# Kernel tuning notes

Hardware: AMD Instinct MI355X
Metric: run time of the kernel (lower is better)

The kernel has to match this reference:

```python
import jax, jax.numpy as jnp
import numpy as np

Q_DIM = 1024
KV_DIM = 1024
D_ATTN = 1024
N_HEADS = 16
HDIM = D_ATTN // N_HEADS
LOOKBACK = 3
KW = LOOKBACK + 1
SCALE = HDIM ** -0.5

B, LQ, LKV = 4, 4096, 512


def setup_inputs() -> dict:
    key = jax.random.key(0)
    ks = jax.random.split(key, 6)
    q = jax.random.normal(ks[0], (B, LQ, Q_DIM), dtype=jnp.float32)
    kv_src = jax.random.normal(ks[1], (B, LKV, KV_DIM), dtype=jnp.float32)
    seg_id = jnp.sort(jax.random.randint(ks[2], (B, LQ), 0, LKV), axis=-1)
    # Linear weights (torch convention: y = x @ W.T), no bias
    Wq = jax.random.normal(ks[3], (D_ATTN, Q_DIM), dtype=jnp.float32) * (Q_DIM ** -0.5)
    Wkv = jax.random.normal(ks[4], (2 * D_ATTN, KV_DIM), dtype=jnp.float32) * (KV_DIM ** -0.5)
    Wo = jax.random.normal(ks[5], (Q_DIM, D_ATTN), dtype=jnp.float32) * (D_ATTN ** -0.5)
    return {"q": q, "kv_src": kv_src, "seg_id": seg_id, "Wq": Wq, "Wkv": Wkv, "Wo": Wo}


def _split_heads(x):
    # (B, L, D) -> (B, H, L, Dh)
    b, l, _ = x.shape
    return x.reshape(b, l, N_HEADS, HDIM).transpose(0, 2, 1, 3)


def reference(q, kv_src, seg_id, Wq, Wkv, Wo):
    b, lq, _ = q.shape
    lkv = kv_src.shape[1]

    qh = _split_heads(q @ Wq.T)                      # (B,H,Lq,Dh)
    kv = kv_src @ Wkv.T                              # (B,Lkv,2*D)
    k, v = jnp.split(kv, 2, axis=-1)
    kh = _split_heads(k)                             # (B,H,Lkv,Dh)
    vh = _split_heads(v)

    offsets = jnp.arange(KW)                         # (Kw,)
    gather = seg_id[:, :, None] - offsets            # (B,Lq,Kw)
    neg_mask = gather < 0
    gc = jnp.clip(gather, 0, lkv - 1)                # (B,Lq,Kw)

    b_idx = jnp.arange(b)[:, None, None]
    # advanced indexing: (B,Lq,Kw,H,Dh) -> transpose to (B,H,Lq,Kw,Dh)
    k_sel = kh[b_idx, :, gc].transpose(0, 3, 1, 2, 4)
    v_sel = vh[b_idx, :, gc].transpose(0, 3, 1, 2, 4)

    scores = jnp.einsum('bhqd,bhqkd->bhqk', qh, k_sel) * SCALE
    neg_inf = jnp.finfo(scores.dtype).min
    scores = jnp.where(neg_mask[:, None, :, :], neg_inf, scores)
    probs = jax.nn.softmax(scores, axis=-1)
    out = jnp.einsum('bhqk,bhqkd->bhqd', probs, v_sel)   # (B,H,Lq,Dh)
    out = out.transpose(0, 2, 1, 3).reshape(b, lq, D_ATTN)
    return out @ Wo.T                                # (B,Lq,q_dim)
```

## Files before the change

### kernel.cpp

```cpp
#include <hip/hip_runtime.h>
#include <math.h>

#define NH 16
#define HDIM 64
#define D_ATTN 1024
#define KW 4
#define ATT_SCALE 0.125f
#define LKV_C 512
#define LQ_C 4096
#define B_C 4

typedef _Float16 f16;
typedef _Float16 f16x8 __attribute__((ext_vector_type(8)));
typedef _Float16 f16x4 __attribute__((ext_vector_type(4)));
typedef float f32x4 __attribute__((ext_vector_type(4)));

typedef __attribute__((address_space(3))) unsigned int as3_uint;
typedef __attribute__((address_space(1))) const unsigned int as1_uint;

__device__ __forceinline__ void gld_lds16(const f16* g, f16* l) {
    __builtin_amdgcn_global_load_lds((as1_uint*)g, (as3_uint*)l, 16, 0, 0);
}

__global__ __launch_bounds__(256) void split_hi(const float* __restrict__ x,
                                                f16* __restrict__ hi, int n4) {
    int i = blockIdx.x * 256 + threadIdx.x;
    if (i >= n4) return;
    float4 v = ((const float4*)x)[i];
    ((f16x4*)hi)[i] = (f16x4){(f16)v.x, (f16)v.y, (f16)v.z, (f16)v.w};
}

template <typename OT>
__global__ __launch_bounds__(256) void gemm_f16(const f16* __restrict__ A,
                                                const f16* __restrict__ B,
                                                OT* __restrict__ C,
                                                int M, int N, int K) {
    __shared__ f16 smem[2 * 128 * 32];
    f16* sA = smem;
    f16* sB = smem + 4096;

    const int t = threadIdx.x;
    const int w = t >> 6;
    const int lane = t & 63;
    const int bm = blockIdx.y * 128;
    const int bn = blockIdx.x * 128;
    const int wm = (w & 1) * 64;
    const int wn = (w >> 1) * 64;

    f32x4 acc[4][4] = {};

    const int frow = lane & 15;
    const int fchunk = lane >> 4;

    const int srow = t >> 2;
    const int chunk = (t & 3) ^ ((t >> 3) & 3);
    const size_t aoff0 = (size_t)(bm + srow) * K + chunk * 8;
    const size_t aoff1 = (size_t)(bm + 64 + srow) * K + chunk * 8;
    const size_t boff0 = (size_t)(bn + srow) * K + chunk * 8;
    const size_t boff1 = (size_t)(bn + 64 + srow) * K + chunk * 8;
    const unsigned loff0 = (w * 64) * 8;
    const unsigned loff1 = (256 + w * 64) * 8;

    gld_lds16(A + aoff0, sA + loff0);  gld_lds16(A + aoff1, sA + loff1);
    gld_lds16(B + boff0, sB + loff0);  gld_lds16(B + boff1, sB + loff1);

    for (int k0 = 0; k0 < K; k0 += 32) {
        __syncthreads();

        f16x8 a[4], b[4];
        #pragma unroll
        for (int i = 0; i < 4; ++i) {
            const int r = wm + i * 16 + frow;
            a[i] = *(const f16x8*)(sA + r * 32 + (fchunk ^ ((r >> 1) & 3)) * 8);
        }
        #pragma unroll
        for (int j = 0; j < 4; ++j) {
            const int r = wn + j * 16 + frow;
            b[j] = *(const f16x8*)(sB + r * 32 + (fchunk ^ ((r >> 1) & 3)) * 8);
        }

        __syncthreads();

        if (k0 + 32 < K) {
            const int kn = k0 + 32;
            gld_lds16(A + aoff0 + kn, sA + loff0);  gld_lds16(A + aoff1 + kn, sA + loff1);
            gld_lds16(B + boff0 + kn, sB + loff0);  gld_lds16(B + boff1 + kn, sB + loff1);
        }

        #pragma unroll
        for (int i = 0; i < 4; ++i)
            #pragma unroll
            for (int j = 0; j < 4; ++j)
                acc[i][j] = __builtin_amdgcn_mfma_f32_16x16x32_f16(a[i], b[j], acc[i][j], 0, 0, 0);
    }

    const int rbase = bm + wm + (lane >> 4) * 4;
    const int cbase = bn + wn + (lane & 15);
    #pragma unroll
    for (int i = 0; i < 4; ++i)
        #pragma unroll
        for (int j = 0; j < 4; ++j)
            #pragma unroll
            for (int r = 0; r < 4; ++r)
                C[(size_t)(rbase + i * 16 + r) * N + cbase + j * 16] = (OT)acc[i][j][r];
}

__device__ __forceinline__ void stage_half(const f16* __restrict__ g, size_t row0,
                                           int K, int kcol, f16* l) {
    const int t = threadIdx.x;
    #pragma unroll
    for (int i = 0; i < 2; ++i) {
        const int idx = i * 512 + t;
        const int r = idx >> 3;
        const int qg = (idx & 7) ^ (r & 7);
        gld_lds16(g + (row0 + r) * (size_t)K + kcol + qg * 8, l + idx * 8);
    }
}

#define BAR __builtin_amdgcn_s_barrier()
#define VM6 asm volatile("s_waitcnt vmcnt(6)" ::: "memory")
#define VM8 asm volatile("s_waitcnt vmcnt(8)" ::: "memory")
#define VM0 asm volatile("s_waitcnt vmcnt(0)" ::: "memory")

#define RD_A(S, mh)                                                         \
    { _Pragma("unroll") for (int mi = 0; mi < 4; ++mi) {                    \
        const f16* p = (S) + ((mh) * 128 + mi * 32 + arow) * 64;            \
        a[0][mi] = *(const f16x8*)(p + q0);                                 \
        a[1][mi] = *(const f16x8*)(p + q1); } }

#define RD_B(S, nh)                                                         \
    { _Pragma("unroll") for (int ni = 0; ni < 2; ++ni) {                    \
        const f16* p = (S) + (((nh) * 2 + ni) * 64 + brow) * 64;            \
        b[0][(nh) * 2 + ni] = *(const f16x8*)(p + q0);                      \
        b[1][(nh) * 2 + ni] = *(const f16x8*)(p + q1); } }

#define QUAD(mh, nh)                                                        \
    { __builtin_amdgcn_s_setprio(1);                                        \
      _Pragma("unroll") for (int mi = 0; mi < 4; ++mi)                      \
      _Pragma("unroll") for (int ni = 0; ni < 2; ++ni) {                    \
          f32x4& c = acc[(mh) * 4 + mi][(nh) * 2 + ni];                     \
          c = __builtin_amdgcn_mfma_f32_16x16x32_f16(a[0][mi], b[0][(nh) * 2 + ni], c, 0, 0, 0); \
          c = __builtin_amdgcn_mfma_f32_16x16x32_f16(a[1][mi], b[1][(nh) * 2 + ni], c, 0, 0, 0); \
      }                                                                     \
      __builtin_amdgcn_s_setprio(0); }

template <typename OT>
__global__ __launch_bounds__(512, 2) void gemm256(const f16* __restrict__ A,
                                                  const f16* __restrict__ B,
                                                  OT* __restrict__ C,
                                                  int M, int N, int K) {
    __shared__ __align__(16) f16 smem[4 * 16384];
    f16* const sA0 = smem;
    f16* const sA1 = smem + 16384;
    f16* const sB0 = smem + 32768;
    f16* const sB1 = smem + 49152;

    const int t = threadIdx.x;
    const int lane = t & 63;
    const int w = t >> 6;
    const int wr = w >> 2;
    const int wc = w & 3;
    const int frow = lane & 15;
    const int fc = lane >> 4;

    const int nbx = N >> 8;
    const int nwg = gridDim.x;
    const int wg = (blockIdx.x & 7) * (nwg >> 3) + (blockIdx.x >> 3);
    const int bm = (wg / nbx) << 8;
    const int bn = (wg % nbx) << 8;

    const int arow = wr * 16 + frow;
    const int brow = wc * 16 + frow;
    const int q0 = (fc ^ (frow & 7)) * 8;
    const int q1 = ((4 + fc) ^ (frow & 7)) * 8;

    f32x4 acc[8][4] = {};
    f16x8 a[2][4], b[2][4];

    stage_half(A, bm,       K, 0,  sA0);
    stage_half(B, bn,       K, 0,  sB0);
    stage_half(B, bn + 128, K, 0,  sB0 + 8192);
    stage_half(A, bm + 128, K, 0,  sA0 + 8192);
    stage_half(A, bm,       K, 64, sA1);
    stage_half(B, bn,       K, 64, sB1);
    stage_half(B, bn + 128, K, 64, sB1 + 8192);
    stage_half(A, bm + 128, K, 64, sA1 + 8192);
    VM8;
    BAR;

    const int NT = K >> 7;
    for (int it = 0; it < NT; ++it) {
        const bool lastit = (it == NT - 1);
        const int kc2 = (it * 2 + 2) << 6;
        const int kc3 = (it * 2 + 3) << 6;

        RD_A(sA0, 0); RD_B(sB0, 0);
        BAR; QUAD(0, 0); BAR;
        RD_B(sB0, 1);
        if (!lastit) { stage_half(A, bm, K, kc2, sA0); stage_half(B, bn, K, kc2, sB0); }
        BAR; QUAD(0, 1); BAR;
        RD_A(sA0, 1);
        if (!lastit) stage_half(B, bn + 128, K, kc2, sB0 + 8192);
        BAR; QUAD(1, 0); BAR;
        if (lastit) { VM0; } else { VM6; stage_half(A, bm + 128, K, kc2, sA0 + 8192); }
        BAR; QUAD(1, 1); BAR;

        RD_A(sA1, 0); RD_B(sB1, 0);
        BAR; QUAD(0, 0); BAR;
        RD_B(sB1, 1);
        if (!lastit) { stage_half(A, bm, K, kc3, sA1); stage_half(B, bn, K, kc3, sB1); }
        BAR; QUAD(0, 1); BAR;
        RD_A(sA1, 1);
        if (!lastit) stage_half(B, bn + 128, K, kc3, sB1 + 8192);
        BAR; QUAD(1, 0); BAR;
        if (!lastit) { VM6; stage_half(A, bm + 128, K, kc3, sA1 + 8192); }
        BAR; QUAD(1, 1); BAR;
    }

    const size_t rb = (size_t)bm + wr * 16 + ((lane >> 4) << 2);
    const int cb = bn + wc * 16 + (lane & 15);
    #pragma unroll
    for (int m = 0; m < 8; ++m)
        #pragma unroll
        for (int n = 0; n < 4; ++n)
            #pragma unroll
            for (int rr = 0; rr < 4; ++rr)
                C[(rb + m * 32 + rr) * N + cb + n * 64] = (OT)acc[m][n][rr];
}

__global__ __launch_bounds__(256) void attn_kernel(const f16* __restrict__ qh,
                                                   const f16* __restrict__ kvp,
                                                   const int* __restrict__ seg_id,
                                                   f16* __restrict__ attn_o) {
    const int hg = threadIdx.x >> 6;
    const int lane = threadIdx.x & 63;
    const int r0 = blockIdx.x << 2;
    const int hh = lane >> 4;
    const int s  = lane & 15;
    const int dbase = (hg * 4 + hh) * HDIM + 4 * s;
    const int b = r0 >> 12;
    const f16* kvb = kvp + (size_t)b * LKV_C * (2 * D_ATTN);

    int seg[4];
    float4 q[4];
    #pragma unroll
    for (int i = 0; i < 4; ++i) {
        seg[i] = seg_id[r0 + i];
        f16x4 qv = *(const f16x4*)(qh + (size_t)(r0 + i) * D_ATTN + dbase);
        q[i] = make_float4((float)qv.x, (float)qv.y, (float)qv.z, (float)qv.w);
    }

    float sc[4][KW];
    #pragma unroll
    for (int i = 0; i < 4; ++i)
        #pragma unroll
        for (int w = 0; w < KW; ++w) {
            const int j = seg[i] - w;
            float p = 0.f;
            if (j >= 0) {
                f16x4 k4 = *(const f16x4*)(kvb + (size_t)j * (2 * D_ATTN) + dbase);
                p = q[i].x * (float)k4.x + q[i].y * (float)k4.y +
                    q[i].z * (float)k4.z + q[i].w * (float)k4.w;
            }
            sc[i][w] = p;
        }
    #pragma unroll
    for (int i = 0; i < 4; ++i)
        #pragma unroll
        for (int w = 0; w < KW; ++w) {
            float p = sc[i][w];
            p += __shfl_xor(p, 1);
            p += __shfl_xor(p, 2);
            p += __shfl_xor(p, 4);
            p += __shfl_xor(p, 8);
            sc[i][w] = (seg[i] - w >= 0) ? p * ATT_SCALE : -1e30f;
        }

    #pragma unroll
    for (int i = 0; i < 4; ++i) {
        const float m = fmaxf(fmaxf(sc[i][0], sc[i][1]), fmaxf(sc[i][2], sc[i][3]));
        float e[KW], sum = 0.f;
        #pragma unroll
        for (int w = 0; w < KW; ++w) {
            e[w] = __expf(sc[i][w] - m);
            sum += e[w];
        }
        const float inv = 1.f / sum;

        float4 o = make_float4(0.f, 0.f, 0.f, 0.f);
        #pragma unroll
        for (int w = 0; w < KW; ++w) {
            const int j = seg[i] - w;
            if (j >= 0) {
                f16x4 v4 = *(const f16x4*)(kvb + (size_t)j * (2 * D_ATTN) + D_ATTN + dbase);
                const float c = e[w] * inv;
                o.x = fmaf(c, (float)v4.x, o.x);
                o.y = fmaf(c, (float)v4.y, o.y);
                o.z = fmaf(c, (float)v4.z, o.z);
                o.w = fmaf(c, (float)v4.w, o.w);
            }
        }
        *(f16x4*)(attn_o + (size_t)(r0 + i) * D_ATTN + dbase) =
            (f16x4){(f16)o.x, (f16)o.y, (f16)o.z, (f16)o.w};
    }
}

extern "C" void kernel_launch(void* const* d_in, const int* in_sizes, int n_in,
                              void* d_out, int out_size, void* d_ws, size_t ws_size,
                              hipStream_t stream) {
    const float* q      = (const float*)d_in[0];
    const float* kv_src = (const float*)d_in[1];
    const int*   seg    = (const int*)  d_in[2];
    const float* Wq     = (const float*)d_in[3];
    const float* Wkv    = (const float*)d_in[4];
    const float* Wo     = (const float*)d_in[5];
    float* out = (float*)d_out;

    const int M  = B_C * LQ_C;
    const int Mk = B_C * LKV_C;

    f16* q_hi   = (f16*)d_ws;
    f16* kvs_hi = q_hi   + (size_t)M * D_ATTN;
    f16* Wq_hi  = kvs_hi + (size_t)Mk * 1024;
    f16* Wkv_hi = Wq_hi  + 1024 * 1024;
    f16* Wo_hi  = Wkv_hi + 2048 * 1024;
    f16* kvp    = Wo_hi  + 1024 * 1024;
    f16* attn_o = q_hi;
    f16* qh16   = (f16*)d_out;

    split_hi<<<(M * D_ATTN) / 1024, 256, 0, stream>>>(q, q_hi, (M * D_ATTN) / 4);
    split_hi<<<(Mk * 1024) / 1024, 256, 0, stream>>>(kv_src, kvs_hi, (Mk * 1024) / 4);
    split_hi<<<(1024 * 1024) / 1024, 256, 0, stream>>>(Wq, Wq_hi, (1024 * 1024) / 4);
    split_hi<<<(2048 * 1024) / 1024, 256, 0, stream>>>(Wkv, Wkv_hi, (2048 * 1024) / 4);
    split_hi<<<(1024 * 1024) / 1024, 256, 0, stream>>>(Wo, Wo_hi, (1024 * 1024) / 4);

    gemm256<f16><<<(M / 256) * (1024 / 256), 512, 0, stream>>>(q_hi, Wq_hi, qh16, M, 1024, 1024);
    gemm_f16<f16><<<dim3(2048 / 128, Mk / 128), 256, 0, stream>>>(kvs_hi, Wkv_hi, kvp, Mk, 2048, 1024);
    attn_kernel<<<M / 4, 256, 0, stream>>>(qh16, kvp, seg, attn_o);
    gemm256<float><<<(M / 256) * (1024 / 256), 512, 0, stream>>>(attn_o, Wo_hi, out, M, 1024, 1024);
}
```

Before: 271.8 us.

## Fuse fp16 conversion launches and restructure gemm256 pipeline into two-quad phases

Replaces five separate fp32-to-fp16 conversion launches with a single segmented kernel, reducing launch overhead and tail effects. The 256x256 GEMM main loop is reorganized so each phase reads a full A half and both B halves, then runs two quads under one priority bump, with global-to-LDS staging regrouped and one A-half stage deferred to the next iteration. The KV projection GEMM is launched before the Q projection. The new staging order changes which loads are outstanding at each wait, which risks stalls or hazards if the vmcnt counts no longer match.

```diff
diff --git a/kernel.cpp b/kernel.cpp
--- a/kernel.cpp
+++ b/kernel.cpp
@@ -22,12 +22,32 @@
     __builtin_amdgcn_global_load_lds((as1_uint*)g, (as3_uint*)l, 16, 0, 0);
 }
 
-__global__ __launch_bounds__(256) void split_hi(const float* __restrict__ x,
-                                                f16* __restrict__ hi, int n4) {
-    int i = blockIdx.x * 256 + threadIdx.x;
-    if (i >= n4) return;
-    float4 v = ((const float4*)x)[i];
-    ((f16x4*)hi)[i] = (f16x4){(f16)v.x, (f16)v.y, (f16)v.z, (f16)v.w};
+#define SEG_Q   4194304
+#define SEG_KV  (SEG_Q + 524288)
+#define SEG_WQ  (SEG_KV + 262144)
+#define SEG_WKV (SEG_WQ + 524288)
+#define SEG_END (SEG_WKV + 262144)
+
+__global__ __launch_bounds__(256) void split_all(const float* __restrict__ q,
+                                                 const float* __restrict__ kv,
+                                                 const float* __restrict__ Wq,
+                                                 const float* __restrict__ Wkv,
+                                                 const float* __restrict__ Wo,
+                                                 f16* __restrict__ q_hi,
+                                                 f16* __restrict__ kvs_hi,
+                                                 f16* __restrict__ Wq_hi,
+                                                 f16* __restrict__ Wkv_hi,
+                                                 f16* __restrict__ Wo_hi) {
+    const int i = blockIdx.x * 256 + threadIdx.x;
+    const float* src; f16* dst; int base;
+    if (i < SEG_Q)        { src = q;   dst = q_hi;   base = 0; }
+    else if (i < SEG_KV)  { src = kv;  dst = kvs_hi; base = SEG_Q; }
+    else if (i < SEG_WQ)  { src = Wq;  dst = Wq_hi;  base = SEG_KV; }
+    else if (i < SEG_WKV) { src = Wkv; dst = Wkv_hi; base = SEG_WQ; }
+    else                  { src = Wo;  dst = Wo_hi;  base = SEG_WKV; }
+    const int j = i - base;
+    float4 v = ((const float4*)src)[j];
+    ((f16x4*)dst)[j] = (f16x4){(f16)v.x, (f16)v.y, (f16)v.z, (f16)v.w};
 }
 
 template <typename OT>
@@ -135,13 +155,15 @@
         b[1][(nh) * 2 + ni] = *(const f16x8*)(p + q1); } }
 
 #define QUAD(mh, nh)                                                        \
-    { __builtin_amdgcn_s_setprio(1);                                        \
-      _Pragma("unroll") for (int mi = 0; mi < 4; ++mi)                      \
+    { _Pragma("unroll") for (int mi = 0; mi < 4; ++mi)                      \
       _Pragma("unroll") for (int ni = 0; ni < 2; ++ni) {                    \
           f32x4& c = acc[(mh) * 4 + mi][(nh) * 2 + ni];                     \
           c = __builtin_amdgcn_mfma_f32_16x16x32_f16(a[0][mi], b[0][(nh) * 2 + ni], c, 0, 0, 0); \
           c = __builtin_amdgcn_mfma_f32_16x16x32_f16(a[1][mi], b[1][(nh) * 2 + ni], c, 0, 0, 0); \
-      }                                                                     \
+      } }
+
+#define QUAD2(mh)                                                           \
+    { __builtin_amdgcn_s_setprio(1); QUAD(mh, 0); QUAD(mh, 1);              \
       __builtin_amdgcn_s_setprio(0); }
 
 template <typename OT>
@@ -191,30 +213,37 @@
     const int NT = K >> 7;
     for (int it = 0; it < NT; ++it) {
         const bool lastit = (it == NT - 1);
+        const int kc1 = (it * 2 + 1) << 6;
         const int kc2 = (it * 2 + 2) << 6;
         const int kc3 = (it * 2 + 3) << 6;
 
-        RD_A(sA0, 0); RD_B(sB0, 0);
-        BAR; QUAD(0, 0); BAR;
-        RD_B(sB0, 1);
-        if (!lastit) { stage_half(A, bm, K, kc2, sA0); stage_half(B, bn, K, kc2, sB0); }
-        BAR; QUAD(0, 1); BAR;
+        RD_A(sA0, 0); RD_B(sB0, 0); RD_B(sB0, 1);
+        if (it > 0) stage_half(A, bm + 128, K, kc1, sA1 + 8192);
+        BAR; QUAD2(0); BAR;
+
         RD_A(sA0, 1);
-        if (!lastit) stage_half(B, bn + 128, K, kc2, sB0 + 8192);
-        BAR; QUAD(1, 0); BAR;
-        if (lastit) { VM0; } else { VM6; stage_half(A, bm + 128, K, kc2, sA0 + 8192); }
-        BAR; QUAD(1, 1); BAR;
-
-        RD_A(sA1, 0); RD_B(sB1, 0);
-        BAR; QUAD(0, 0); BAR;
-        RD_B(sB1, 1);
-        if (!lastit) { stage_half(A, bm, K, kc3, sA1); stage_half(B, bn, K, kc3, sB1); }
-        BAR; QUAD(0, 1); BAR;
+        if (!lastit) {
+            stage_half(A, bm,       K, kc2, sA0);
+            stage_half(B, bn,       K, kc2, sB0);
+            stage_half(B, bn + 128, K, kc2, sB0 + 8192);
+            VM6;
+        } else {
+            VM0;
+        }
+        BAR; QUAD2(1); BAR;
+
+        RD_A(sA1, 0); RD_B(sB1, 0); RD_B(sB1, 1);
+        if (!lastit) stage_half(A, bm + 128, K, kc2, sA0 + 8192);
+        BAR; QUAD2(0); BAR;
+
         RD_A(sA1, 1);
-        if (!lastit) stage_half(B, bn + 128, K, kc3, sB1 + 8192);
-        BAR; QUAD(1, 0); BAR;
-        if (!lastit) { VM6; stage_half(A, bm + 128, K, kc3, sA1 + 8192); }
-        BAR; QUAD(1, 1); BAR;
+        if (!lastit) {
+            stage_half(A, bm,       K, kc3, sA1);
+            stage_half(B, bn,       K, kc3, sB1);
+            stage_half(B, bn + 128, K, kc3, sB1 + 8192);
+            VM6;
+        }
+        BAR; QUAD2(1); BAR;
     }
 
     const size_t rb = (size_t)bm + wr * 16 + ((lane >> 4) << 2);
@@ -328,14 +357,11 @@
     f16* attn_o = q_hi;
     f16* qh16   = (f16*)d_out;
 
-    split_hi<<<(M * D_ATTN) / 1024, 256, 0, stream>>>(q, q_hi, (M * D_ATTN) / 4);
-    split_hi<<<(Mk * 1024) / 1024, 256, 0, stream>>>(kv_src, kvs_hi, (Mk * 1024) / 4);
-    split_hi<<<(1024 * 1024) / 1024, 256, 0, stream>>>(Wq, Wq_hi, (1024 * 1024) / 4);
-    split_hi<<<(2048 * 1024) / 1024, 256, 0, stream>>>(Wkv, Wkv_hi, (2048 * 1024) / 4);
-    split_hi<<<(1024 * 1024) / 1024, 256, 0, stream>>>(Wo, Wo_hi, (1024 * 1024) / 4);
-
+    split_all<<<SEG_END / 256, 256, 0, stream>>>(q, kv_src, Wq, Wkv, Wo,
+                                                 q_hi, kvs_hi, Wq_hi, Wkv_hi, Wo_hi);
+
+    gemm_f16<f16><<<dim3(2048 / 128, Mk / 128), 256, 0, stream>>>(kvs_hi, Wkv_hi, kvp, Mk, 2048, 1024);
     gemm256<f16><<<(M / 256) * (1024 / 256), 512, 0, stream>>>(q_hi, Wq_hi, qh16, M, 1024, 1024);
-    gemm_f16<f16><<<dim3(2048 / 128, Mk / 128), 256, 0, stream>>>(kvs_hi, Wkv_hi, kvp, Mk, 2048, 1024);
     attn_kernel<<<M / 4, 256, 0, stream>>>(qh16, kvp, seg, attn_o);
     gemm256<float><<<(M / 256) * (1024 / 256), 512, 0, stream>>>(attn_o, Wo_hi, out, M, 1024, 1024);
 }
```

New measurement: 266.5 us. No clear change (-1.9%).
